# Performance work log

Measured on AMD Instinct MI355X. Metric: run time of the kernel, lower is better.

## Reference

```python
import jax, jax.numpy as jnp
import numpy as np

B, L, H, W = 64, 512, 768, 255


def setup_inputs() -> dict:
    key = jax.random.key(0)
    k1, k2 = jax.random.split(key)
    sequence_output = jax.random.normal(k1, (B, L, H), dtype=jnp.float32)
    # subword lengths in {1,2}; W=255 guarantees cumsum <= 510 <= L-1 (CLS at pos 0)
    words_lengths = jax.random.randint(k2, (B, W), 1, 3, dtype=jnp.int32)
    return {"sequence_output": sequence_output, "words_lengths": words_lengths}


def reference(sequence_output, words_lengths):
    # sequence_output: [B, L, H] (BERT last_hidden_state after dropout=identity in eval)
    # words_lengths:   [B, W] number of subword tokens per word (0 => padding word)
    Bv, Lv, Hv = sequence_output.shape
    Wv = words_lengths.shape[1]

    cls_output = sequence_output[:, 0, :]  # [B, H]

    # word w occupies tokens [starts[w], ends[w]) with starts = 1 + cumsum - len
    ends = 1 + jnp.cumsum(words_lengths, axis=1)  # [B, W]
    tok = jnp.arange(Lv)                          # [L]

    # token t belongs to word i iff ends[i-1] <= t < ends[i]; zero-length words are
    # skipped automatically by searchsorted(side='right') on the nondecreasing ends.
    word_id = jax.vmap(lambda e: jnp.searchsorted(e, tok, side="right"))(ends)  # [B, L]

    valid = (tok[None, :] >= 1) & (word_id < Wv)  # exclude [CLS] and tokens past last word
    seg_id = jnp.where(valid, word_id, Wv)        # dump invalid tokens into segment W

    sums = jax.vmap(
        lambda x, s: jax.ops.segment_sum(x, s, num_segments=Wv + 1)
    )(sequence_output, seg_id)[:, :Wv]            # [B, W, H]

    denom = jnp.maximum(words_lengths, 1).astype(sequence_output.dtype)  # avoid /0
    context_embedding = sums / denom[..., None]
    context_embedding = jnp.where(
        (words_lengths > 0)[..., None], context_embedding, jnp.zeros((), sums.dtype)
    )
    return cls_output, context_embedding
```

## Files before the change

kernel.cpp:

```cpp
#include <hip/hip_runtime.h>

#define B_ 64
#define L_ 512
#define H_ 768
#define W_ 255
#define H4 (H_ / 4)
#define WPB 16
#define NCHUNK 16

__global__ __launch_bounds__(H4) void wordrep_fused(
        const float* __restrict__ seq,
        const int* __restrict__ lengths,
        float* __restrict__ cls_out,
        float* __restrict__ ctx_out) {
    int chunk = blockIdx.x;
    int b     = blockIdx.y;
    int t     = threadIdx.x;
    const float4* base = (const float4*)(seq + (size_t)b * L_ * H_);

    if (chunk == NCHUNK) {
        ((float4*)cls_out)[(size_t)b * H4 + t] = base[t];
        return;
    }

    int w0 = chunk * WPB;
    int nw = min(WPB, W_ - w0);
    int lane = t & 63;
    const int* len = lengths + b * W_;

    int myStart = 0, myLen = 0;
    int carry = 1;
    int lim = w0 + nw;
    for (int basew = 0; basew < lim; basew += 64) {
        int i = basew + lane;
        int v = (i < lim) ? len[i] : 0;
        int s = v;
        #pragma unroll
        for (int off = 1; off < 64; off <<= 1) {
            int u = __shfl_up(s, off, 64);
            if (lane >= off) s += u;
        }
        if (i >= w0 && i < lim) { myStart = carry + (s - v); myLen = v; }
        carry += __shfl(s, 63, 64);
    }

    int srcBase = w0 & 63;
    float4* out = (float4*)ctx_out + ((size_t)b * W_ + w0) * H4 + t;

    #pragma unroll 4
    for (int j = 0; j < nw; ++j) {
        int sj = __shfl(myStart, srcBase + j, 64);
        int lj = __shfl(myLen,  srcBase + j, 64);
        float4 acc = make_float4(0.f, 0.f, 0.f, 0.f);
        if (lj > 0) {
            int end = sj + lj;
            if (end > L_) end = L_;
            for (int tok = sj; tok < end; ++tok) {
                float4 v = base[(size_t)tok * H4 + t];
                acc.x += v.x; acc.y += v.y; acc.z += v.z; acc.w += v.w;
            }
            float inv = 1.0f / (float)lj;
            acc.x *= inv; acc.y *= inv; acc.z *= inv; acc.w *= inv;
        }
        out[(size_t)j * H4] = acc;
    }
}

extern "C" void kernel_launch(void* const* d_in, const int* in_sizes, int n_in,
                              void* d_out, int out_size, void* d_ws, size_t ws_size,
                              hipStream_t stream) {
    const float* seq     = (const float*)d_in[0];
    const int*   lengths = (const int*)d_in[1];

    float* cls_out = (float*)d_out;
    float* ctx_out = (float*)d_out + (size_t)B_ * H_;

    dim3 grid(NCHUNK + 1, B_);
    wordrep_fused<<<grid, H4, 0, stream>>>(seq, lengths, cls_out, ctx_out);
}
```

Baseline: 162.2 us.

## Batch-prefetch first two tokens per word and halve words per block

Each block now handles 8 words instead of 16, which doubles the grid in the chunk dimension. All loads for the first two tokens of every word in the chunk are issued up front into register arrays, so the gathers are in flight together instead of serialized per word. The rest of each word is handled by the remaining loop, which runs only for lengths above two. This raises memory-level parallelism and block count, at the cost of more registers, redundant loads for length-1 words, and an extra prefix-scan per block.

```diff
diff --git a/kernel.cpp b/kernel.cpp
--- a/kernel.cpp
+++ b/kernel.cpp
@@ -5,8 +5,8 @@
 #define H_ 768
 #define W_ 255
 #define H4 (H_ / 4)
-#define WPB 16
-#define NCHUNK 16
+#define WPB 8
+#define NCHUNK 32
 
 __global__ __launch_bounds__(H4) void wordrep_fused(
         const float* __restrict__ seq,
@@ -45,24 +45,45 @@
     }
 
     int srcBase = w0 & 63;
+
+    int s_[WPB], l_[WPB];
+    #pragma unroll
+    for (int j = 0; j < WPB; ++j) {
+        s_[j] = __shfl(myStart, srcBase + j, 64);
+        l_[j] = __shfl(myLen,   srcBase + j, 64);
+    }
+
+    float4 a0[WPB], a1[WPB];
+    #pragma unroll
+    for (int j = 0; j < WPB; ++j) {
+        int t0 = min(max(s_[j], 0), L_ - 1);
+        int t1 = min(max(s_[j] + (l_[j] > 1 ? 1 : 0), 0), L_ - 1);
+        a0[j] = base[(size_t)t0 * H4 + t];
+        a1[j] = base[(size_t)t1 * H4 + t];
+    }
+
     float4* out = (float4*)ctx_out + ((size_t)b * W_ + w0) * H4 + t;
 
-    #pragma unroll 4
-    for (int j = 0; j < nw; ++j) {
-        int sj = __shfl(myStart, srcBase + j, 64);
-        int lj = __shfl(myLen,  srcBase + j, 64);
-        float4 acc = make_float4(0.f, 0.f, 0.f, 0.f);
-        if (lj > 0) {
-            int end = sj + lj;
-            if (end > L_) end = L_;
-            for (int tok = sj; tok < end; ++tok) {
+    #pragma unroll
+    for (int j = 0; j < WPB; ++j) {
+        int lj = l_[j];
+        float m1 = (lj > 1) ? 1.0f : 0.0f;
+        float4 acc;
+        acc.x = a0[j].x + m1 * a1[j].x;
+        acc.y = a0[j].y + m1 * a1[j].y;
+        acc.z = a0[j].z + m1 * a1[j].z;
+        acc.w = a0[j].w + m1 * a1[j].w;
+        if (lj > 2) {
+            int end = min(s_[j] + lj, L_);
+            for (int tok = s_[j] + 2; tok < end; ++tok) {
                 float4 v = base[(size_t)tok * H4 + t];
                 acc.x += v.x; acc.y += v.y; acc.z += v.z; acc.w += v.w;
             }
-            float inv = 1.0f / (float)lj;
-            acc.x *= inv; acc.y *= inv; acc.z *= inv; acc.w *= inv;
         }
-        out[(size_t)j * H4] = acc;
+        float inv = (lj > 0) ? (1.0f / (float)lj) : 0.0f;
+        acc.x *= inv; acc.y *= inv; acc.z *= inv; acc.w *= inv;
+        if (lj <= 0) { acc.x = 0.f; acc.y = 0.f; acc.z = 0.f; acc.w = 0.f; }
+        if (j < nw) out[(size_t)j * H4] = acc;
     }
 }
 
```

New measurement: 159.1 us. Within noise of the previous version (-1.9%).
